# Kernel optimization log

Measured on AMD Instinct MI355X. Metric: run time of the kernel, lower is better.

Reference implementation:

```python
import itertools
import jax, jax.numpy as jnp
import numpy as np

B = 8192          # batch
V = 100000        # vocab per field
D = 64            # emb_dim
NUM_DENSE = 15    # categorical fields, input shape [B,1] each
SEQ_LEN = 50      # sequence field length
F = NUM_DENSE + 1 # total fields after concat
HID = 30          # deep_layer_size

_pairs = list(itertools.combinations(range(F), 2))  # 120 pairs
ROWS = jnp.array([p[0] for p in _pairs], dtype=jnp.int32)
COLS = jnp.array([p[1] for p in _pairs], dtype=jnp.int32)
PAIR_NUM = len(_pairs)


def setup_inputs() -> dict:
    key = jax.random.key(0)
    ks = jax.random.split(key, 9)
    dense_ids = jax.random.randint(ks[0], (B, NUM_DENSE), 0, V, dtype=jnp.int32)
    seq_ids = jax.random.randint(ks[1], (B, SEQ_LEN), 0, V, dtype=jnp.int32)
    # per-field embedding tables (stacked for the 15 categorical fields)
    tables_dense = jax.random.normal(ks[2], (NUM_DENSE, V, D), dtype=jnp.float32) * 0.01
    table_seq = jax.random.normal(ks[3], (V, D), dtype=jnp.float32) * 0.01
    inner_w = jax.random.normal(ks[4], (PAIR_NUM, D), dtype=jnp.float32) * 0.01
    in_dim = F * D + PAIR_NUM  # lz (flattened embeddings) + lp (pairwise products)
    W1 = jax.random.normal(ks[5], (in_dim, HID), dtype=jnp.float32) * 0.05
    b1 = jnp.zeros((HID,), dtype=jnp.float32)
    W2 = jax.random.normal(ks[6], (HID, 1), dtype=jnp.float32) * 0.05
    b2 = jnp.zeros((1,), dtype=jnp.float32)
    return {"dense_ids": dense_ids, "seq_ids": seq_ids,
            "tables_dense": tables_dense, "table_seq": table_seq,
            "inner_w": inner_w, "W1": W1, "b1": b1, "W2": W2, "b2": b2}


def reference(dense_ids, seq_ids, tables_dense, table_seq, inner_w, W1, b1, W2, b2):
    # per-field embedding lookup: [B, NUM_DENSE, D]
    emb_dense = tables_dense[jnp.arange(NUM_DENSE)[None, :], dense_ids]
    # sequence field: lookup then mean over time (keepdims -> field axis): [B, 1, D]
    emb_seq = jnp.mean(table_seq[seq_ids], axis=1, keepdims=True)
    emb = jnp.concatenate([emb_dense, emb_seq], axis=1)  # [B, F, D]
    lz = emb.reshape(B, F * D)
    # pairwise field gathers (inner product layer)
    p = emb[:, ROWS]                                    # [B, P, D]
    q = emb[:, COLS]                                    # [B, P, D]
    lp = jnp.sum(p * q * inner_w[None], axis=-1)        # [B, P]
    h = jax.nn.relu(jnp.concatenate([lz, lp], axis=1) @ W1 + b1)
    return jax.nn.sigmoid(h @ W2 + b2)                  # [B, 1]
```

## Files before the change

### kernel.cpp

```cpp
#include <hip/hip_runtime.h>

#define NB 8192
#define VV 100000
#define DD 64
#define ND 15
#define SL 50
#define FF 16
#define HH 30
#define PN 120

__constant__ unsigned char pair_rc[PN] = {
    1,2,3,4,5,6,7,8,9,10,11,12,13,14,15,
    18,19,20,21,22,23,24,25,26,27,28,29,30,31,
    35,36,37,38,39,40,41,42,43,44,45,46,47,
    52,53,54,55,56,57,58,59,60,61,62,63,
    69,70,71,72,73,74,75,76,77,78,79,
    86,87,88,89,90,91,92,93,94,95,
    103,104,105,106,107,108,109,110,111,
    120,121,122,123,124,125,126,127,
    137,138,139,140,141,142,143,
    154,155,156,157,158,159,
    171,172,173,174,175,
    188,189,190,191,
    205,206,207,
    222,223,
    239
};

__global__ __launch_bounds__(256) void pnn_fused(
    const int* __restrict__ dense_ids, const int* __restrict__ seq_ids,
    const float* __restrict__ tables_dense, const float* __restrict__ table_seq,
    const float* __restrict__ inner_w, const float* __restrict__ W1,
    const float* __restrict__ b1, const float* __restrict__ W2,
    const float* __restrict__ b2, float* __restrict__ out)
{
    __shared__ float X[4][1152];

    const int wave = threadIdx.x >> 6;
    const int lane = threadIdx.x & 63;
    const int s = (blockIdx.x << 2) | wave;

    {
        const int d = lane;
        float e[FF];
        const int* dp = dense_ids + s * ND;
        #pragma unroll
        for (int f = 0; f < ND; ++f) {
            int id = dp[f];
            e[f] = tables_dense[((size_t)f * VV + id) * DD + d];
        }
        float a0 = 0.0f, a1 = 0.0f;
        const int* sp = seq_ids + s * SL;
        #pragma unroll 5
        for (int i = 0; i < SL; i += 2) {
            int id0 = sp[i];
            int id1 = sp[i + 1];
            a0 += table_seq[(size_t)id0 * DD + d];
            a1 += table_seq[(size_t)id1 * DD + d];
        }
        e[15] = (a0 + a1) * (1.0f / SL);
        #pragma unroll
        for (int f = 0; f < FF; ++f) X[wave][f * DD + d] = e[f];
    }
    __syncthreads();

    #pragma unroll
    for (int pp = 0; pp < 2; ++pp) {
        int p = lane + pp * 64;
        if (p < PN) {
            int rc = pair_rc[p];
            const float* er = &X[wave][(rc >> 4) * DD];
            const float* ec = &X[wave][(rc & 15) * DD];
            const float* w  = inner_w + p * DD;
            float acc = 0.0f;
            #pragma unroll 4
            for (int i = 0; i < DD; ++i) {
                int d = (i + lane) & (DD - 1);
                acc = fmaf(er[d] * ec[d], w[d], acc);
            }
            X[wave][FF * DD + p] = acc;
        }
    }
    __syncthreads();

    const int j = lane & 31;
    const int half = lane >> 5;
    float acc = 0.0f;
    if (j < HH) {
        const int kbase = half * 572;
        const float* xp = &X[wave][kbase];
        const float* w1 = W1 + j;
        #pragma unroll 4
        for (int k = 0; k < 572; ++k)
            acc = fmaf(xp[k], w1[(size_t)(kbase + k) * HH], acc);
    }
    acc += __shfl_xor(acc, 32);

    float t = 0.0f;
    if (lane < HH) t = fmaxf(acc + b1[lane], 0.0f) * W2[lane];
    #pragma unroll
    for (int off = 16; off > 0; off >>= 1) t += __shfl_xor(t, off);

    if (lane == 0) {
        float z = t + b2[0];
        out[s] = 1.0f / (1.0f + __expf(-z));
    }
}

extern "C" void kernel_launch(void* const* d_in, const int* in_sizes, int n_in,
                              void* d_out, int out_size, void* d_ws, size_t ws_size,
                              hipStream_t stream) {
    const int* dense_ids    = (const int*)d_in[0];
    const int* seq_ids      = (const int*)d_in[1];
    const float* tables_dense = (const float*)d_in[2];
    const float* table_seq    = (const float*)d_in[3];
    const float* inner_w      = (const float*)d_in[4];
    const float* W1           = (const float*)d_in[5];
    const float* b1           = (const float*)d_in[6];
    const float* W2           = (const float*)d_in[7];
    const float* b2           = (const float*)d_in[8];

    pnn_fused<<<NB / 4, 256, 0, stream>>>(
        dense_ids, seq_ids, tables_dense, table_seq,
        inner_w, W1, b1, W2, b2, (float*)d_out);
}
```

Before: 546.7 us.

## Rewrite PNN kernel with bf16 MFMA for W1 GEMM and 16-sample blocks

Splits the work into a prep kernel that transposes W1 and packs it to bf16, and a main kernel that handles 16 samples per block. Embeddings are gathered with float2 loads into a swizzled bf16 shared buffer. Pair products reuse inner_w held in registers across 8 samples, and the dense layer runs as a 16x16x32 bf16 MFMA instead of scalar FMAs over fp32 W1. The intent is to stop every sample re-reading W1 from global memory and to use matrix cores. In exchange, embeddings, pair products and W1 all lose precision by going to bf16, and the W1 conversion runs on every call.

```diff
diff --git a/kernel.cpp b/kernel.cpp
--- a/kernel.cpp
+++ b/kernel.cpp
@@ -1,15 +1,19 @@
 #include <hip/hip_runtime.h>
 
-#define NB 8192
 #define VV 100000
 #define DD 64
 #define ND 15
 #define SL 50
-#define FF 16
 #define HH 30
 #define PN 120
-
-__constant__ unsigned char pair_rc[PN] = {
+#define KX 1152
+#define SPB 16
+#define XROWB 2320
+
+typedef __attribute__((ext_vector_type(8))) short short8;
+typedef __attribute__((ext_vector_type(4))) float f32x4;
+
+__constant__ unsigned char pair_rc[128] = {
     1,2,3,4,5,6,7,8,9,10,11,12,13,14,15,
     18,19,20,21,22,23,24,25,26,27,28,29,30,31,
     35,36,37,38,39,40,41,42,43,44,45,46,47,
@@ -24,94 +28,177 @@
     188,189,190,191,
     205,206,207,
     222,223,
-    239
+    239,
+    0,0,0,0,0,0,0,0
 };
 
-__global__ __launch_bounds__(256) void pnn_fused(
+__device__ __forceinline__ unsigned short f2bf(float x) {
+    unsigned u = __float_as_uint(x);
+    u += 0x7fffu + ((u >> 16) & 1u);
+    return (unsigned short)(u >> 16);
+}
+__device__ __forceinline__ float bflo(unsigned u) { return __uint_as_float(u << 16); }
+__device__ __forceinline__ float bfhi(unsigned u) { return __uint_as_float(u & 0xffff0000u); }
+
+__global__ __launch_bounds__(256) void prep_w1t(const float* __restrict__ W1,
+                                                unsigned* __restrict__ w1t) {
+    int u = blockIdx.x * 256 + threadIdx.x;
+    int n = u / 576;
+    int k2 = u - n * 576;
+    int k = k2 * 2;
+    float v0 = (n < HH && k < 1144) ? W1[(size_t)k * HH + n] : 0.f;
+    float v1 = (n < HH && (k + 1) < 1144) ? W1[(size_t)(k + 1) * HH + n] : 0.f;
+    w1t[u] = (unsigned)f2bf(v0) | ((unsigned)f2bf(v1) << 16);
+}
+
+__global__ __launch_bounds__(256) void pnn_main(
     const int* __restrict__ dense_ids, const int* __restrict__ seq_ids,
     const float* __restrict__ tables_dense, const float* __restrict__ table_seq,
-    const float* __restrict__ inner_w, const float* __restrict__ W1,
+    const float* __restrict__ inner_w, const unsigned short* __restrict__ w1t,
     const float* __restrict__ b1, const float* __restrict__ W2,
     const float* __restrict__ b2, float* __restrict__ out)
 {
-    __shared__ float X[4][1152];
-
-    const int wave = threadIdx.x >> 6;
-    const int lane = threadIdx.x & 63;
-    const int s = (blockIdx.x << 2) | wave;
-
-    {
-        const int d = lane;
-        float e[FF];
-        const int* dp = dense_ids + s * ND;
+    __shared__ __align__(16) unsigned char Xraw[SPB * XROWB];
+    __shared__ int ids_d[SPB * ND];
+    __shared__ int ids_s[SPB * SL];
+    __shared__ float red[4 * SPB * 32];
+
+    const int t = threadIdx.x;
+    const int wave = t >> 6;
+    const int lane = t & 63;
+    const int sbase = blockIdx.x * SPB;
+
+    if (t < SPB * ND) ids_d[t] = dense_ids[sbase * ND + t];
+    for (int i = t; i < SPB * SL; i += 256) ids_s[i] = seq_ids[sbase * SL + i];
+    __syncthreads();
+
+    {
+        const int half = lane >> 5;
+        const int dl = (lane & 31) * 2;
+        for (int si = 0; si < 4; ++si) {
+            const int sl_ = wave * 4 + si;
+            #pragma unroll
+            for (int i = 0; i < 8; ++i) {
+                int f = 2 * i + half;
+                if (f < ND) {
+                    int id = ids_d[sl_ * ND + f];
+                    float2 v = *(const float2*)(tables_dense + ((size_t)f * VV + id) * DD + dl);
+                    unsigned pk = (unsigned)f2bf(v.x) | ((unsigned)f2bf(v.y) << 16);
+                    int k = f * DD + dl;
+                    int ch = (k >> 3) ^ (f & 7);
+                    *(unsigned*)(&Xraw[sl_ * XROWB + ch * 16 + (dl & 7) * 2]) = pk;
+                }
+            }
+            float a0 = 0.f, a1 = 0.f;
+            const int* sid = &ids_s[sl_ * SL];
+            #pragma unroll 5
+            for (int i = 0; i < 25; ++i) {
+                int id = sid[2 * i + half];
+                float2 v = *(const float2*)(table_seq + (size_t)id * DD + dl);
+                a0 += v.x; a1 += v.y;
+            }
+            a0 += __shfl_xor(a0, 32);
+            a1 += __shfl_xor(a1, 32);
+            if (half == 0) {
+                unsigned pk = (unsigned)f2bf(a0 * 0.02f) | ((unsigned)f2bf(a1 * 0.02f) << 16);
+                int k = 15 * DD + dl;
+                int ch = (k >> 3) ^ 7;
+                *(unsigned*)(&Xraw[sl_ * XROWB + ch * 16 + (dl & 7) * 2]) = pk;
+            }
+        }
+    }
+    __syncthreads();
+
+    {
+        const int p = t & 127;
+        const int sg = t >> 7;
+        const bool valid = p < PN;
+        const int rc = pair_rc[p];
+        const int r = rc >> 4, c = rc & 15;
+        f32x4 w4[16];
+        if (valid) {
+            const float* wp = inner_w + p * DD;
+            #pragma unroll
+            for (int i = 0; i < 16; ++i) w4[i] = *(const f32x4*)(wp + i * 4);
+        }
+        #pragma unroll 2
+        for (int si = 0; si < 8; ++si) {
+            const int sl_ = sg * 8 + si;
+            float acc = 0.f;
+            if (valid) {
+                #pragma unroll
+                for (int ch = 0; ch < 8; ++ch) {
+                    int cr = (r * 8 + ch) ^ (r & 7);
+                    int cc = (c * 8 + ch) ^ (c & 7);
+                    uint4 xr = *(const uint4*)(&Xraw[sl_ * XROWB + cr * 16]);
+                    uint4 xc = *(const uint4*)(&Xraw[sl_ * XROWB + cc * 16]);
+                    acc = fmaf(bflo(xr.x) * bflo(xc.x), w4[ch * 2].x, acc);
+                    acc = fmaf(bfhi(xr.x) * bfhi(xc.x), w4[ch * 2].y, acc);
+                    acc = fmaf(bflo(xr.y) * bflo(xc.y), w4[ch * 2].z, acc);
+                    acc = fmaf(bfhi(xr.y) * bfhi(xc.y), w4[ch * 2].w, acc);
+                    acc = fmaf(bflo(xr.z) * bflo(xc.z), w4[ch * 2 + 1].x, acc);
+                    acc = fmaf(bfhi(xr.z) * bfhi(xc.z), w4[ch * 2 + 1].y, acc);
+                    acc = fmaf(bflo(xr.w) * bflo(xc.w), w4[ch * 2 + 1].z, acc);
+                    acc = fmaf(bfhi(xr.w) * bfhi(xc.w), w4[ch * 2 + 1].w, acc);
+                }
+            }
+            int k = 1024 + p;
+            int ch = (k >> 3) ^ ((k >> 6) & 7);
+            *(unsigned short*)(&Xraw[sl_ * XROWB + ch * 16 + (p & 7) * 2]) = f2bf(acc);
+        }
+    }
+    __syncthreads();
+
+    {
+        const int m = lane & 15;
+        const int kg = lane >> 4;
+        f32x4 acc0 = {0.f, 0.f, 0.f, 0.f}, acc1 = {0.f, 0.f, 0.f, 0.f};
         #pragma unroll
-        for (int f = 0; f < ND; ++f) {
-            int id = dp[f];
-            e[f] = tables_dense[((size_t)f * VV + id) * DD + d];
-        }
-        float a0 = 0.0f, a1 = 0.0f;
-        const int* sp = seq_ids + s * SL;
-        #pragma unroll 5
-        for (int i = 0; i < SL; i += 2) {
-            int id0 = sp[i];
-            int id1 = sp[i + 1];
-            a0 += table_seq[(size_t)id0 * DD + d];
-            a1 += table_seq[(size_t)id1 * DD + d];
-        }
-        e[15] = (a0 + a1) * (1.0f / SL);
+        for (int i = 0; i < 9; ++i) {
+            int kt = wave * 9 + i;
+            int k = kt * 32 + kg * 8;
+            int ch = (kt * 4 + kg) ^ ((kt >> 1) & 7);
+            short8 a  = *(const short8*)(&Xraw[m * XROWB + ch * 16]);
+            short8 b0 = *(const short8*)(w1t + (size_t)m * KX + k);
+            short8 b1 = *(const short8*)(w1t + (size_t)(m + 16) * KX + k);
+            acc0 = __builtin_amdgcn_mfma_f32_16x16x32_bf16(a, b0, acc0, 0, 0, 0);
+            acc1 = __builtin_amdgcn_mfma_f32_16x16x32_bf16(a, b1, acc1, 0, 0, 0);
+        }
         #pragma unroll
-        for (int f = 0; f < FF; ++f) X[wave][f * DD + d] = e[f];
-    }
-    __syncthreads();
-
-    #pragma unroll
-    for (int pp = 0; pp < 2; ++pp) {
-        int p = lane + pp * 64;
-        if (p < PN) {
-            int rc = pair_rc[p];
-            const float* er = &X[wave][(rc >> 4) * DD];
-            const float* ec = &X[wave][(rc & 15) * DD];
-            const float* w  = inner_w + p * DD;
-            float acc = 0.0f;
-            #pragma unroll 4
-            for (int i = 0; i < DD; ++i) {
-                int d = (i + lane) & (DD - 1);
-                acc = fmaf(er[d] * ec[d], w[d], acc);
-            }
-            X[wave][FF * DD + p] = acc;
-        }
-    }
-    __syncthreads();
-
-    const int j = lane & 31;
-    const int half = lane >> 5;
-    float acc = 0.0f;
-    if (j < HH) {
-        const int kbase = half * 572;
-        const float* xp = &X[wave][kbase];
-        const float* w1 = W1 + j;
-        #pragma unroll 4
-        for (int k = 0; k < 572; ++k)
-            acc = fmaf(xp[k], w1[(size_t)(kbase + k) * HH], acc);
-    }
-    acc += __shfl_xor(acc, 32);
-
-    float t = 0.0f;
-    if (lane < HH) t = fmaxf(acc + b1[lane], 0.0f) * W2[lane];
-    #pragma unroll
-    for (int off = 16; off > 0; off >>= 1) t += __shfl_xor(t, off);
-
-    if (lane == 0) {
-        float z = t + b2[0];
-        out[s] = 1.0f / (1.0f + __expf(-z));
+        for (int reg = 0; reg < 4; ++reg) {
+            int smp = kg * 4 + reg;
+            red[wave * 512 + smp * 32 + m] = acc0[reg];
+            red[wave * 512 + smp * 32 + 16 + m] = acc1[reg];
+        }
+    }
+    __syncthreads();
+
+    {
+        float w2v = (lane < HH) ? W2[lane] : 0.f;
+        float b1v = (lane < HH) ? b1[lane] : 0.f;
+        for (int si = 0; si < 4; ++si) {
+            int sl_ = wave * 4 + si;
+            float v = 0.f;
+            if (lane < HH) {
+                v = red[0 * 512 + sl_ * 32 + lane] + red[1 * 512 + sl_ * 32 + lane]
+                  + red[2 * 512 + sl_ * 32 + lane] + red[3 * 512 + sl_ * 32 + lane];
+                v = fmaxf(v + b1v, 0.f) * w2v;
+            }
+            #pragma unroll
+            for (int off = 32; off > 0; off >>= 1) v += __shfl_xor(v, off);
+            if (lane == 0) {
+                float z = v + b2[0];
+                out[sbase + sl_] = 1.f / (1.f + __expf(-z));
+            }
+        }
     }
 }
 
 extern "C" void kernel_launch(void* const* d_in, const int* in_sizes, int n_in,
                               void* d_out, int out_size, void* d_ws, size_t ws_size,
                               hipStream_t stream) {
-    const int* dense_ids    = (const int*)d_in[0];
-    const int* seq_ids      = (const int*)d_in[1];
+    const int* dense_ids      = (const int*)d_in[0];
+    const int* seq_ids        = (const int*)d_in[1];
     const float* tables_dense = (const float*)d_in[2];
     const float* table_seq    = (const float*)d_in[3];
     const float* inner_w      = (const float*)d_in[4];
@@ -120,7 +207,8 @@
     const float* W2           = (const float*)d_in[7];
     const float* b2           = (const float*)d_in[8];
 
-    pnn_fused<<<NB / 4, 256, 0, stream>>>(
-        dense_ids, seq_ids, tables_dense, table_seq,
-        inner_w, W1, b1, W2, b2, (float*)d_out);
-}
+    prep_w1t<<<72, 256, 0, stream>>>(W1, (unsigned*)d_ws);
+    pnn_main<<<512, 256, 0, stream>>>(dense_ids, seq_ids, tables_dense, table_seq,
+                                      inner_w, (const unsigned short*)d_ws,
+                                      b1, W2, b2, (float*)d_out);
+}
```

Measured after the change: 473.2 us. 13.5% less time.
